# Kernel tuning notes

Hardware: AMD Instinct MI355X
Metric: run time of the kernel (lower is better)

Reference implementation:

```python
import jax, jax.numpy as jnp
import numpy as np

TEMP = 1.0  # temperature

def setup_inputs() -> dict:
    key = jax.random.key(0)
    ks = jax.random.split(key, 16)
    B, Cin, Cout, H, W, K, kk, A = 32, 64, 64, 128, 128, 4, 3, 16
    c_ = Cin + Cout
    r = lambda k, s: jax.random.normal(k, s, dtype=jnp.float32)
    return {
        'x': r(ks[0], (B, Cin, H, W)),
        'fc_w': r(ks[1], (A, Cin)) * 0.1,
        'ch_w': r(ks[2], (Cin, A)) * 0.1,
        'ch_b': jnp.zeros((Cin,), jnp.float32),
        'f_w': r(ks[3], (Cout, A)) * 0.1,
        'f_b': jnp.zeros((Cout,), jnp.float32),
        'sp_w': r(ks[4], (kk * kk, A)) * 0.1,
        'sp_b': jnp.zeros((kk * kk,), jnp.float32),
        'k_w': r(ks[5], (K, A)) * 0.1,
        'k_b': jnp.zeros((K,), jnp.float32),
        'fus_w1': r(ks[6], (c_ // 16, c_)) * 0.1,
        'fus_b1': jnp.zeros((c_ // 16,), jnp.float32),
        'fus_w2': r(ks[7], (c_, c_ // 16)) * 0.1,
        'fus_b2': jnp.zeros((c_,), jnp.float32),
        'weight': r(ks[8], (K, Cout, Cin, kk, kk)) * (1.0 / np.sqrt(Cin * kk * kk)),
    }

def reference(x, fc_w, ch_w, ch_b, f_w, f_b, sp_w, sp_b, k_w, k_b,
              fus_w1, fus_b1, fus_w2, fus_b2, weight):
    B, Cin, H, W = x.shape
    K, Cout, _, kk, _ = weight.shape
    # --- Attention branches (on globally pooled features) ---
    pooled = x.mean(axis=(2, 3))                      # (B, Cin)
    a = jax.nn.relu(pooled @ fc_w.T)                  # (B, A)
    ch_att = jax.nn.sigmoid(a @ ch_w.T + ch_b)        # (B, Cin)
    f_att = jax.nn.sigmoid(a @ f_w.T + f_b)           # (B, Cout)
    sp_att = jax.nn.sigmoid(a @ sp_w.T + sp_b).reshape(B, 1, 1, 1, kk, kk)
    k_att = jax.nn.softmax((a @ k_w.T + k_b) / TEMP, axis=1).reshape(B, K, 1, 1, 1, 1)
    # --- Attention fusion ---
    att = jnp.concatenate([ch_att, f_att], axis=1)    # (B, Cin+Cout)
    att2 = jax.nn.sigmoid(jax.nn.relu(att @ fus_w1.T + fus_b1) @ fus_w2.T + fus_b2)
    s1 = att2[:, :Cin].sum(axis=1)
    s2 = att2[:, Cin:].sum(axis=1)
    score = jax.nn.softmax(jnp.stack([s1, s2], axis=1) / TEMP, axis=1)
    w1 = score[:, 0][:, None, None, None]
    w2 = score[:, 1][:, None, None, None]
    # --- Apply channel attention, aggregate per-sample weights ---
    xm = w1 * x * ch_att[:, :, None, None]
    # (B,K,1,1,kk,kk)*(B,K,1,1,1,1)*(1,K,Cout,Cin,kk,kk) summed over K
    agg_w = (sp_att * k_att * weight[None]).sum(axis=1)  # (B, Cout, Cin, kk, kk)
    # --- Per-sample conv2d (stride 1, padding 1) ---
    def conv_one(xb, wb):
        return jax.lax.conv_general_dilated(
            xb[None], wb, window_strides=(1, 1), padding=[(1, 1), (1, 1)],
            dimension_numbers=('NCHW', 'OIHW', 'NCHW'))[0]
    out = jax.vmap(conv_one)(xm, agg_w)               # (B, Cout, H, W)
    return w2 * out * f_att[:, :, None, None]
```

## Files before the change

### kernel.cpp

```cpp
#include <hip/hip_runtime.h>
#include <math.h>
#include <stdint.h>

typedef short bf16x8 __attribute__((ext_vector_type(8)));
typedef float f32x16 __attribute__((ext_vector_type(16)));
typedef unsigned short ushort_t;

#define WS_POOLED 0
#define WS_CIN    2048
#define WS_COUT   4096
#define WS_SP9    6144
#define WS_K4     6432
#define WS_WF     8192

static __device__ __forceinline__ unsigned f2bf(float f) {
  unsigned u = __builtin_bit_cast(unsigned, f);
  return (u + 0x7FFFu + ((u >> 16) & 1u)) >> 16;
}
static __device__ __forceinline__ unsigned pk2(float a, float b) {
  return f2bf(a) | (f2bf(b) << 16);
}

__global__ __launch_bounds__(256) void pool_kernel(const float* __restrict__ x,
                                                   float* __restrict__ pooled) {
  const int bc = blockIdx.x;
  const int tid = threadIdx.x;
  const float4* p = (const float4*)(x + (size_t)bc * 16384);
  float s = 0.f;
  for (int j = tid; j < 4096; j += 256) {
    float4 v = p[j];
    s += (v.x + v.y) + (v.z + v.w);
  }
#pragma unroll
  for (int off = 32; off > 0; off >>= 1) s += __shfl_down(s, off, 64);
  __shared__ float red[4];
  if ((tid & 63) == 0) red[tid >> 6] = s;
  __syncthreads();
  if (tid == 0) pooled[bc] = (red[0] + red[1] + red[2] + red[3]) * (1.f / 16384.f);
}

__global__ __launch_bounds__(128) void att_kernel(
    const float* __restrict__ pooled,
    const float* __restrict__ fc_w, const float* __restrict__ ch_w, const float* __restrict__ ch_b,
    const float* __restrict__ f_w,  const float* __restrict__ f_b,
    const float* __restrict__ sp_w, const float* __restrict__ sp_b,
    const float* __restrict__ k_w,  const float* __restrict__ k_b,
    const float* __restrict__ fus_w1, const float* __restrict__ fus_b1,
    const float* __restrict__ fus_w2, const float* __restrict__ fus_b2,
    float* __restrict__ o_cin, float* __restrict__ o_cout,
    float* __restrict__ o_sp9, float* __restrict__ o_k4) {
  const int b = blockIdx.x;
  const int t = threadIdx.x;
  __shared__ float s_pool[64], s_a[16], s_att[128], s_sp[9], s_k[4], s_h[8],
      s_att2[128], s_red[2], s_w12[2];

  if (t < 64) s_pool[t] = pooled[b * 64 + t];
  __syncthreads();

  if (t < 16) {
    float s = 0.f;
    for (int c = 0; c < 64; ++c) s += s_pool[c] * fc_w[t * 64 + c];
    s_a[t] = fmaxf(s, 0.f);
  }
  __syncthreads();

  if (t < 64) {
    float s = ch_b[t];
    for (int j = 0; j < 16; ++j) s += s_a[j] * ch_w[t * 16 + j];
    s_att[t] = 1.f / (1.f + expf(-s));
  } else {
    const int o = t - 64;
    float s = f_b[o];
    for (int j = 0; j < 16; ++j) s += s_a[j] * f_w[o * 16 + j];
    s_att[t] = 1.f / (1.f + expf(-s));
  }
  if (t < 9) {
    float s = sp_b[t];
    for (int j = 0; j < 16; ++j) s += s_a[j] * sp_w[t * 16 + j];
    s_sp[t] = 1.f / (1.f + expf(-s));
  }
  if (t < 4) {
    float s = k_b[t];
    for (int j = 0; j < 16; ++j) s += s_a[j] * k_w[t * 16 + j];
    s_k[t] = s;
  }
  __syncthreads();

  if (t < 8) {
    float s = fus_b1[t];
    for (int c = 0; c < 128; ++c) s += s_att[c] * fus_w1[t * 128 + c];
    s_h[t] = fmaxf(s, 0.f);
  }
  if (t == 127) {
    float m = fmaxf(fmaxf(s_k[0], s_k[1]), fmaxf(s_k[2], s_k[3]));
    float e0 = expf(s_k[0] - m), e1 = expf(s_k[1] - m);
    float e2 = expf(s_k[2] - m), e3 = expf(s_k[3] - m);
    float inv = 1.f / (e0 + e1 + e2 + e3);
    s_k[0] = e0 * inv; s_k[1] = e1 * inv; s_k[2] = e2 * inv; s_k[3] = e3 * inv;
  }
  __syncthreads();

  {
    float s = fus_b2[t];
    for (int j = 0; j < 8; ++j) s += s_h[j] * fus_w2[t * 8 + j];
    s_att2[t] = 1.f / (1.f + expf(-s));
  }
  __syncthreads();

  if (t < 2) {
    float s = 0.f;
    for (int c = 0; c < 64; ++c) s += s_att2[t * 64 + c];
    s_red[t] = s;
  }
  __syncthreads();
  if (t == 0) {
    float m = fmaxf(s_red[0], s_red[1]);
    float e1 = expf(s_red[0] - m), e2 = expf(s_red[1] - m);
    float inv = 1.f / (e1 + e2);
    s_w12[0] = e1 * inv;
    s_w12[1] = e2 * inv;
  }
  __syncthreads();

  if (t < 64) {
    o_cin[b * 64 + t]  = s_w12[0] * s_att[t];
    o_cout[b * 64 + t] = s_w12[1] * s_att[64 + t];
  }
  if (t < 9) o_sp9[b * 9 + t] = s_sp[t];
  if (t < 4) o_k4[b * 4 + t] = s_k[t];
}

__global__ __launch_bounds__(256) void wf_kernel(const float* __restrict__ weight,
                                                 const float* __restrict__ cin,
                                                 const float* __restrict__ cout_,
                                                 const float* __restrict__ sp9,
                                                 const float* __restrict__ k4,
                                                 ushort_t* __restrict__ wfb) {
  const int bo = blockIdx.x;
  const int b = bo >> 6, o = bo & 63;
  const float co = cout_[b * 64 + o];
  const float k0 = k4[b * 4 + 0], k1 = k4[b * 4 + 1];
  const float k2 = k4[b * 4 + 2], k3 = k4[b * 4 + 3];
  for (int idx = threadIdx.x; idx < 576; idx += 256) {
    const int pq = idx >> 6, i = idx & 63;
    const size_t wi = ((size_t)o * 64 + i) * 9 + pq;
    float s = k0 * weight[wi] + k1 * weight[36864 + wi] +
              k2 * weight[73728 + wi] + k3 * weight[110592 + wi];
    float v = co * sp9[b * 9 + pq] * cin[b * 64 + i] * s;
    wfb[((size_t)(b * 9 + pq) * 64 + o) * 64 + i] = (ushort_t)f2bf(v);
  }
}

#define CONV_BUF_BYTES 26112
__global__ __launch_bounds__(256, 2) void conv_kernel(const float* __restrict__ x,
                                                      const ushort_t* __restrict__ wfb,
                                                      float* __restrict__ out) {
  const int b  = blockIdx.x >> 5;
  const int h0 = (blockIdx.x & 31) << 2;
  const int tid = threadIdx.x;
  const int lane = tid & 63;
  const int wv  = tid >> 6;
  const int l31 = lane & 31;
  const int hi  = lane >> 5;

  __shared__ __align__(16) short sx[2 * 816 * 16];

  f32x16 acc[2][4];
#pragma unroll
  for (int of = 0; of < 2; ++of)
#pragma unroll
    for (int nt = 0; nt < 4; ++nt)
#pragma unroll
      for (int r = 0; r < 16; ++r) acc[of][nt][r] = 0.f;

  const ushort_t* wfb_b = wfb + (size_t)b * 9 * 64 * 64;

  const bool sact = tid < 204;
  const int sr = tid / 34, sc = tid % 34;
  const int gr  = h0 - 1 + sr;
  const int gcb = sc * 4 - 4;
  const bool inb = sact && ((unsigned)gr < 128u) && ((unsigned)gcb < 128u);
  const int pixb = sr * 136 + sc * 4;
  const int key = (tid & 7) << 4;
  const float* xrow = x + ((size_t)b * 64) * 16384 + gr * 128 + gcb;

#define PACK_WRITE(BUFB)                                                        \
  do {                                                                          \
    _Pragma("unroll") for (int oct = 0; oct < 2; ++oct) {                       \
      _Pragma("unroll") for (int j = 0; j < 4; ++j) {                           \
        uint4 u;                                                                \
        u.x = pk2(((const float*)&v[oct * 8 + 0])[j], ((const float*)&v[oct * 8 + 1])[j]); \
        u.y = pk2(((const float*)&v[oct * 8 + 2])[j], ((const float*)&v[oct * 8 + 3])[j]); \
        u.z = pk2(((const float*)&v[oct * 8 + 4])[j], ((const float*)&v[oct * 8 + 5])[j]); \
        u.w = pk2(((const float*)&v[oct * 8 + 6])[j], ((const float*)&v[oct * 8 + 7])[j]); \
        *(uint4*)((char*)sx + (BUFB) + ((((pixb + j) * 32) + oct * 16) ^ key)) = u; \
      }                                                                         \
    }                                                                           \
  } while (0)

  if (sact && !inb) {
    const uint4 z = make_uint4(0u, 0u, 0u, 0u);
#pragma unroll
    for (int buf = 0; buf < 2; ++buf)
#pragma unroll
      for (int oct = 0; oct < 2; ++oct)
#pragma unroll
        for (int j = 0; j < 4; ++j)
          *(uint4*)((char*)sx + buf * CONV_BUF_BYTES +
                    ((((pixb + j) * 32) + oct * 16) ^ key)) = z;
  }

  float4 v[16];
  if (inb) {
#pragma unroll
    for (int ci = 0; ci < 16; ++ci) v[ci] = *(const float4*)(xrow + (size_t)ci * 16384);
    PACK_WRITE(0);
  }
  __syncthreads();

#pragma unroll
  for (int ch = 0; ch < 4; ++ch) {
    const int c0 = ch * 16;
    if (ch < 3 && inb) {
#pragma unroll
      for (int ci = 0; ci < 16; ++ci)
        v[ci] = *(const float4*)(xrow + (size_t)(c0 + 16 + ci) * 16384);
    }
    const int bufb = (ch & 1) * CONV_BUF_BYTES;
#pragma unroll
    for (int p = 0; p < 3; ++p) {
#pragma unroll
      for (int q = 0; q < 3; ++q) {
        const int tap = p * 3 + q;
        bf16x8 af0 = *(const bf16x8*)(wfb_b + (tap * 64 + l31) * 64 + c0 + hi * 8);
        bf16x8 af1 = *(const bf16x8*)(wfb_b + (tap * 64 + 32 + l31) * 64 + c0 + hi * 8);
#pragma unroll
        for (int nt = 0; nt < 4; ++nt) {
          const int pix = (wv + p) * 136 + 3 + q + nt * 32 + l31;
          const int boff = bufb + ((pix * 32 + hi * 16) ^ (((pix >> 2) & 7) << 4));
          bf16x8 bf = *(const bf16x8*)((const char*)sx + boff);
          acc[0][nt] = __builtin_amdgcn_mfma_f32_32x32x16_bf16(af0, bf, acc[0][nt], 0, 0, 0);
          acc[1][nt] = __builtin_amdgcn_mfma_f32_32x32x16_bf16(af1, bf, acc[1][nt], 0, 0, 0);
        }
      }
    }
    if (ch < 3) {
      if (inb) PACK_WRITE(((ch + 1) & 1) * CONV_BUF_BYTES);
      __syncthreads();
    }
  }

  const int h = h0 + wv;
#pragma unroll
  for (int of = 0; of < 2; ++of) {
#pragma unroll
    for (int nt = 0; nt < 4; ++nt) {
      const int col = nt * 32 + l31;
#pragma unroll
      for (int reg = 0; reg < 16; ++reg) {
        const int o = of * 32 + (reg & 3) + ((reg >> 2) << 3) + (hi << 2);
        out[(((size_t)(b * 64 + o)) * 128 + h) * 128 + col] = acc[of][nt][reg];
      }
    }
  }
#undef PACK_WRITE
}

extern "C" void kernel_launch(void* const* d_in, const int* in_sizes, int n_in,
                              void* d_out, int out_size, void* d_ws, size_t ws_size,
                              hipStream_t stream) {
  const float* x      = (const float*)d_in[0];
  const float* fc_w   = (const float*)d_in[1];
  const float* ch_w   = (const float*)d_in[2];
  const float* ch_b   = (const float*)d_in[3];
  const float* f_w    = (const float*)d_in[4];
  const float* f_b    = (const float*)d_in[5];
  const float* sp_w   = (const float*)d_in[6];
  const float* sp_b   = (const float*)d_in[7];
  const float* k_w    = (const float*)d_in[8];
  const float* k_b    = (const float*)d_in[9];
  const float* fus_w1 = (const float*)d_in[10];
  const float* fus_b1 = (const float*)d_in[11];
  const float* fus_w2 = (const float*)d_in[12];
  const float* fus_b2 = (const float*)d_in[13];
  const float* weight = (const float*)d_in[14];
  float* ws  = (float*)d_ws;
  float* out = (float*)d_out;
  ushort_t* wfb = (ushort_t*)(ws + WS_WF);

  pool_kernel<<<2048, 256, 0, stream>>>(x, ws + WS_POOLED);
  att_kernel<<<32, 128, 0, stream>>>(ws + WS_POOLED, fc_w, ch_w, ch_b, f_w, f_b,
                                     sp_w, sp_b, k_w, k_b, fus_w1, fus_b1,
                                     fus_w2, fus_b2, ws + WS_CIN, ws + WS_COUT,
                                     ws + WS_SP9, ws + WS_K4);
  wf_kernel<<<2048, 256, 0, stream>>>(weight, ws + WS_CIN, ws + WS_COUT,
                                      ws + WS_SP9, ws + WS_K4, wfb);
  conv_kernel<<<1024, 256, 0, stream>>>(x, wfb, out);
}
```

Baseline: 170.1 us.

## Split conv work across 8 waves per block to cut per-thread registers

```diff
diff --git a/kernel.cpp b/kernel.cpp
--- a/kernel.cpp
+++ b/kernel.cpp
@@ -152,68 +152,77 @@
 }
 
 #define CONV_BUF_BYTES 26112
-__global__ __launch_bounds__(256, 2) void conv_kernel(const float* __restrict__ x,
+__global__ __launch_bounds__(512, 4) void conv_kernel(const float* __restrict__ x,
                                                       const ushort_t* __restrict__ wfb,
                                                       float* __restrict__ out) {
   const int b  = blockIdx.x >> 5;
   const int h0 = (blockIdx.x & 31) << 2;
   const int tid = threadIdx.x;
   const int lane = tid & 63;
-  const int wv  = tid >> 6;
+  const int wid = tid >> 6;
+  const int rw    = wid >> 1;
+  const int nhalf = wid & 1;
   const int l31 = lane & 31;
   const int hi  = lane >> 5;
 
   __shared__ __align__(16) short sx[2 * 816 * 16];
 
-  f32x16 acc[2][4];
-#pragma unroll
-  for (int of = 0; of < 2; ++of)
-#pragma unroll
-    for (int nt = 0; nt < 4; ++nt)
-#pragma unroll
-      for (int r = 0; r < 16; ++r) acc[of][nt][r] = 0.f;
+  f32x16 acc00, acc01, acc10, acc11;
+#pragma unroll
+  for (int r = 0; r < 16; ++r) { acc00[r] = 0.f; acc01[r] = 0.f; acc10[r] = 0.f; acc11[r] = 0.f; }
 
   const ushort_t* wfb_b = wfb + (size_t)b * 9 * 64 * 64;
 
-  const bool sact = tid < 204;
-  const int sr = tid / 34, sc = tid % 34;
+  const bool sact = tid < 408;
+  int so = 0, sr = 0, sc = 0;
+  if (sact) { so = tid / 204; const int rem = tid % 204; sr = rem / 34; sc = rem % 34; }
   const int gr  = h0 - 1 + sr;
   const int gcb = sc * 4 - 4;
   const bool inb = sact && ((unsigned)gr < 128u) && ((unsigned)gcb < 128u);
   const int pixb = sr * 136 + sc * 4;
-  const int key = (tid & 7) << 4;
+  const int key = ((pixb >> 2) & 7) << 4;
+  const int oct16 = so * 16;
   const float* xrow = x + ((size_t)b * 64) * 16384 + gr * 128 + gcb;
 
-#define PACK_WRITE(BUFB)                                                        \
-  do {                                                                          \
-    _Pragma("unroll") for (int oct = 0; oct < 2; ++oct) {                       \
-      _Pragma("unroll") for (int j = 0; j < 4; ++j) {                           \
-        uint4 u;                                                                \
-        u.x = pk2(((const float*)&v[oct * 8 + 0])[j], ((const float*)&v[oct * 8 + 1])[j]); \
-        u.y = pk2(((const float*)&v[oct * 8 + 2])[j], ((const float*)&v[oct * 8 + 3])[j]); \
-        u.z = pk2(((const float*)&v[oct * 8 + 4])[j], ((const float*)&v[oct * 8 + 5])[j]); \
-        u.w = pk2(((const float*)&v[oct * 8 + 6])[j], ((const float*)&v[oct * 8 + 7])[j]); \
-        *(uint4*)((char*)sx + (BUFB) + ((((pixb + j) * 32) + oct * 16) ^ key)) = u; \
-      }                                                                         \
-    }                                                                           \
+  float4 v0, v1, v2, v3, v4, v5, v6, v7;
+
+#define LOADV(C0)                                              \
+  do {                                                         \
+    v0 = *(const float4*)(xrow + (size_t)((C0) + 0) * 16384);  \
+    v1 = *(const float4*)(xrow + (size_t)((C0) + 1) * 16384);  \
+    v2 = *(const float4*)(xrow + (size_t)((C0) + 2) * 16384);  \
+    v3 = *(const float4*)(xrow + (size_t)((C0) + 3) * 16384);  \
+    v4 = *(const float4*)(xrow + (size_t)((C0) + 4) * 16384);  \
+    v5 = *(const float4*)(xrow + (size_t)((C0) + 5) * 16384);  \
+    v6 = *(const float4*)(xrow + (size_t)((C0) + 6) * 16384);  \
+    v7 = *(const float4*)(xrow + (size_t)((C0) + 7) * 16384);  \
   } while (0)
+
+#define PKW(J, FLD, BUFB)                                                     \
+  do {                                                                        \
+    uint4 u;                                                                  \
+    u.x = pk2(v0.FLD, v1.FLD);                                                \
+    u.y = pk2(v2.FLD, v3.FLD);                                                \
+    u.z = pk2(v4.FLD, v5.FLD);                                                \
+    u.w = pk2(v6.FLD, v7.FLD);                                                \
+    *(uint4*)((char*)sx + (BUFB) + ((((pixb + (J)) * 32) + oct16) ^ key)) = u;\
+  } while (0)
+
+#define PACK_WRITE(BUFB) \
+  do { PKW(0, x, BUFB); PKW(1, y, BUFB); PKW(2, z, BUFB); PKW(3, w, BUFB); } while (0)
 
   if (sact && !inb) {
     const uint4 z = make_uint4(0u, 0u, 0u, 0u);
 #pragma unroll
     for (int buf = 0; buf < 2; ++buf)
 #pragma unroll
-      for (int oct = 0; oct < 2; ++oct)
-#pragma unroll
-        for (int j = 0; j < 4; ++j)
-          *(uint4*)((char*)sx + buf * CONV_BUF_BYTES +
-                    ((((pixb + j) * 32) + oct * 16) ^ key)) = z;
-  }
-
-  float4 v[16];
+      for (int j = 0; j < 4; ++j)
+        *(uint4*)((char*)sx + buf * CONV_BUF_BYTES +
+                  ((((pixb + j) * 32) + oct16) ^ key)) = z;
+  }
+
   if (inb) {
-#pragma unroll
-    for (int ci = 0; ci < 16; ++ci) v[ci] = *(const float4*)(xrow + (size_t)ci * 16384);
+    LOADV(so * 8);
     PACK_WRITE(0);
   }
   __syncthreads();
@@ -221,11 +230,7 @@
 #pragma unroll
   for (int ch = 0; ch < 4; ++ch) {
     const int c0 = ch * 16;
-    if (ch < 3 && inb) {
-#pragma unroll
-      for (int ci = 0; ci < 16; ++ci)
-        v[ci] = *(const float4*)(xrow + (size_t)(c0 + 16 + ci) * 16384);
-    }
+    if (ch < 3 && inb) LOADV(c0 + 16 + so * 8);
     const int bufb = (ch & 1) * CONV_BUF_BYTES;
 #pragma unroll
     for (int p = 0; p < 3; ++p) {
@@ -234,13 +239,19 @@
         const int tap = p * 3 + q;
         bf16x8 af0 = *(const bf16x8*)(wfb_b + (tap * 64 + l31) * 64 + c0 + hi * 8);
         bf16x8 af1 = *(const bf16x8*)(wfb_b + (tap * 64 + 32 + l31) * 64 + c0 + hi * 8);
-#pragma unroll
-        for (int nt = 0; nt < 4; ++nt) {
-          const int pix = (wv + p) * 136 + 3 + q + nt * 32 + l31;
+        {
+          const int pix = (rw + p) * 136 + 3 + q + nhalf * 64 + l31;
           const int boff = bufb + ((pix * 32 + hi * 16) ^ (((pix >> 2) & 7) << 4));
           bf16x8 bf = *(const bf16x8*)((const char*)sx + boff);
-          acc[0][nt] = __builtin_amdgcn_mfma_f32_32x32x16_bf16(af0, bf, acc[0][nt], 0, 0, 0);
-          acc[1][nt] = __builtin_amdgcn_mfma_f32_32x32x16_bf16(af1, bf, acc[1][nt], 0, 0, 0);
+          acc00 = __builtin_amdgcn_mfma_f32_32x32x16_bf16(af0, bf, acc00, 0, 0, 0);
+          acc10 = __builtin_amdgcn_mfma_f32_32x32x16_bf16(af1, bf, acc10, 0, 0, 0);
+        }
+        {
+          const int pix = (rw + p) * 136 + 3 + q + nhalf * 64 + 32 + l31;
+          const int boff = bufb + ((pix * 32 + hi * 16) ^ (((pix >> 2) & 7) << 4));
+          bf16x8 bf = *(const bf16x8*)((const char*)sx + boff);
+          acc01 = __builtin_amdgcn_mfma_f32_32x32x16_bf16(af0, bf, acc01, 0, 0, 0);
+          acc11 = __builtin_amdgcn_mfma_f32_32x32x16_bf16(af1, bf, acc11, 0, 0, 0);
         }
       }
     }
@@ -250,20 +261,24 @@
     }
   }
 
-  const int h = h0 + wv;
-#pragma unroll
-  for (int of = 0; of < 2; ++of) {
-#pragma unroll
-    for (int nt = 0; nt < 4; ++nt) {
-      const int col = nt * 32 + l31;
-#pragma unroll
-      for (int reg = 0; reg < 16; ++reg) {
-        const int o = of * 32 + (reg & 3) + ((reg >> 2) << 3) + (hi << 2);
-        out[(((size_t)(b * 64 + o)) * 128 + h) * 128 + col] = acc[of][nt][reg];
-      }
-    }
-  }
+  const int h = h0 + rw;
+#define STORE_ACC(ACC, OFB, NT)                                                \
+  do {                                                                         \
+    const int col = nhalf * 64 + (NT) * 32 + l31;                              \
+    _Pragma("unroll") for (int reg = 0; reg < 16; ++reg) {                     \
+      const int o = (OFB) + (reg & 3) + ((reg >> 2) << 3) + (hi << 2);         \
+      out[(((size_t)(b * 64 + o)) * 128 + h) * 128 + col] = (ACC)[reg];        \
+    }                                                                          \
+  } while (0)
+
+  STORE_ACC(acc00, 0, 0);
+  STORE_ACC(acc01, 0, 1);
+  STORE_ACC(acc10, 32, 0);
+  STORE_ACC(acc11, 32, 1);
+#undef STORE_ACC
 #undef PACK_WRITE
+#undef PKW
+#undef LOADV
 }
 
 extern "C" void kernel_launch(void* const* d_in, const int* in_sizes, int n_in,
@@ -295,5 +310,5 @@
                                      ws + WS_SP9, ws + WS_K4);
   wf_kernel<<<2048, 256, 0, stream>>>(weight, ws + WS_CIN, ws + WS_COUT,
                                       ws + WS_SP9, ws + WS_K4, wfb);
-  conv_kernel<<<1024, 256, 0, stream>>>(x, wfb, out);
-}
+  conv_kernel<<<1024, 512, 0, stream>>>(x, wfb, out);
+}
```

After: 168.9 us. About the same (-0.7%).
